# Kernel optimization log

Hardware: AMD Instinct MI355X
Metric: run time of the kernel (lower is better)

The kernel has to match this reference:

```python
import jax, jax.numpy as jnp
from jax import lax
import numpy as np


def _lap(cost):
    """Jonker-Volgenant shortest-augmenting-path LAP (same optimum as
    scipy.optimize.linear_sum_assignment) on cost [n, m] with n <= m.
    Returns for each row (0..n-1) the assigned column index."""
    n, m = cost.shape
    BIG = jnp.asarray(1e9, cost.dtype)
    a = jnp.pad(cost, ((1, 0), (1, 0)))  # 1-based rows/cols, [n+1, m+1]
    u = jnp.zeros(n + 1, cost.dtype)     # row duals
    v = jnp.zeros(m + 1, cost.dtype)     # col duals
    p = jnp.zeros(m + 1, jnp.int32)      # p[j] = row matched to col j (0 = free)

    def row_step(i, carry):
        u, v, p = carry
        p = p.at[0].set(i)  # virtual col 0 holds the row being inserted
        minv = jnp.full(m + 1, BIG, cost.dtype)
        used = jnp.zeros(m + 1, bool)
        way = jnp.zeros(m + 1, jnp.int32)

        def cond(s):
            u, v, p, way, minv, used, j0 = s
            return p[j0] != 0

        def body(s):
            u, v, p, way, minv, used, j0 = s
            used = used.at[j0].set(True)
            i0 = p[j0]
            cur = a[i0] - u[i0] - v                      # reduced costs, len m+1
            better = (cur < minv) & jnp.logical_not(used)
            minv = jnp.where(better, cur, minv)
            way = jnp.where(better, j0, way)
            masked = jnp.where(used, BIG, minv)
            j1 = jnp.argmin(masked).astype(jnp.int32)
            delta = masked[j1]
            u = u.at[p].add(jnp.where(used, delta, jnp.zeros((), cost.dtype)))
            v = jnp.where(used, v - delta, v)
            minv = jnp.where(used, minv, minv - delta)
            return (u, v, p, way, minv, used, j1)

        u, v, p, way, minv, used, j0 = lax.while_loop(
            cond, body, (u, v, p, way, minv, used, jnp.int32(0)))

        # backtrack the augmenting path
        def cond2(s):
            return s[1] != 0

        def body2(s):
            p, j0 = s
            j1 = way[j0]
            return (p.at[j0].set(p[j1]), j1)

        p, _ = lax.while_loop(cond2, body2, (p, j0))
        return (u, v, p)

    u, v, p = lax.fori_loop(1, n + 1, row_step, (u, v, p))
    # invert: row r (1-based) matched to col j  ->  ans[r-1] = j-1
    cols = jnp.arange(m + 1)
    valid = (p > 0) & (cols > 0)
    idx = jnp.where(valid, p - 1, n)  # invalid entries dumped into scratch slot n
    ans = jnp.zeros(n + 1, jnp.int32).at[idx].set((cols - 1).astype(jnp.int32))
    return ans[:n]


def _cdist_mm(x, y):
    """Batched euclidean cdist via the GEMM trick (torch use_mm_for_euclid_dist)."""
    x2 = jnp.sum(x * x, axis=-1)[..., :, None]   # [B, N, 1]
    y2 = jnp.sum(y * y, axis=-1)[..., None, :]   # [B, 1, M]
    xy = jnp.einsum('bnd,bmd->bnm', x, y)        # [B, N, M]
    return jnp.sqrt(jnp.maximum(x2 + y2 - 2.0 * xy, 0.0))


def setup_inputs() -> dict:
    key = jax.random.key(0)
    k1, k2 = jax.random.split(key)
    outputs = jax.random.normal(k1, (32, 512, 768), dtype=jnp.float32)
    targets = jax.random.normal(k2, (32, 200, 768), dtype=jnp.float32)
    return {"outputs": outputs, "targets": targets}


def reference(outputs, targets):
    # cost[b, n, m] = ||outputs[b, n] - targets[b, m]||_2  (block-diagonal slices
    # of the original cross-batch cdist are all that the matcher consumes)
    cost = _cdist_mm(outputs, targets)                       # [B, N, M]
    # solve with targets as rows (n=M <= m=N): pred column per gt row
    gt_to_pred = jax.vmap(_lap)(jnp.swapaxes(cost, 1, 2))    # [B, M]
    # scipy returns pred indices sorted ascending; replicate that ordering
    order = jnp.argsort(gt_to_pred, axis=1)                  # gt indices (index_j)
    index_i = jnp.take_along_axis(gt_to_pred, order, axis=1)
    index_j = order.astype(jnp.int32)
    return jnp.stack([index_i, index_j], axis=1)             # [B, 2, M] int32
```

## Files before the change

kernel.cpp:

```cpp
#include <hip/hip_runtime.h>
#include <math.h>

static constexpr int BATCH = 32;
static constexpr int NPRED = 512;
static constexpr int NTGT  = 200;
static constexpr int DIM   = 768;
#define BIGF  1e9f
#define USEDC 2e9f

__global__ __launch_bounds__(64) void row_norms_kernel(const float* __restrict__ x,
                                                       float* __restrict__ out) {
    int row = blockIdx.x;
    const float4* r = (const float4*)(x + (size_t)row * DIM);
    float s = 0.f;
#pragma unroll
    for (int k = 0; k < 3; ++k) {
        float4 v = r[threadIdx.x + 64 * k];
        s += v.x * v.x + v.y * v.y + v.z * v.z + v.w * v.w;
    }
#pragma unroll
    for (int off = 32; off; off >>= 1) s += __shfl_down(s, off);
    if (threadIdx.x == 0) out[row] = s;
}

__global__ __launch_bounds__(256) void cost_kernel(const float* __restrict__ O,
                                                   const float* __restrict__ T,
                                                   const float* __restrict__ no_arr,
                                                   const float* __restrict__ nt_arr,
                                                   float* __restrict__ cost) {
    const int b  = blockIdx.z;
    const int m0 = blockIdx.y * 32;
    const int n0 = blockIdx.x * 128;
    const float* Tb = T + (size_t)b * NTGT * DIM;
    const float* Ob = O + (size_t)b * NPRED * DIM;

    __shared__ float As[32][33];
    __shared__ float Bs[32][129];

    const int tid = threadIdx.x;
    const int tx = tid & 31;
    const int ty = tid >> 5;

    float acc[4][4] = {};

    for (int k0 = 0; k0 < DIM; k0 += 32) {
        {
            int ar = tid >> 3;
            int ak = (tid & 7) << 2;
            int gm = m0 + ar; if (gm > NTGT - 1) gm = NTGT - 1;
            float4 vA = *(const float4*)(Tb + (size_t)gm * DIM + k0 + ak);
            As[ak + 0][ar] = vA.x; As[ak + 1][ar] = vA.y;
            As[ak + 2][ar] = vA.z; As[ak + 3][ar] = vA.w;
        }
#pragma unroll
        for (int q = 0; q < 4; ++q) {
            int idx = q * 256 + tid;
            int br = idx >> 3;
            int bk = (idx & 7) << 2;
            float4 vB = *(const float4*)(Ob + (size_t)(n0 + br) * DIM + k0 + bk);
            Bs[bk + 0][br] = vB.x; Bs[bk + 1][br] = vB.y;
            Bs[bk + 2][br] = vB.z; Bs[bk + 3][br] = vB.w;
        }
        __syncthreads();
#pragma unroll
        for (int k = 0; k < 32; ++k) {
            float a0 = As[k][ty], a1 = As[k][ty + 8],
                  a2 = As[k][ty + 16], a3 = As[k][ty + 24];
            float b0 = Bs[k][tx],      b1 = Bs[k][tx + 32],
                  b2 = Bs[k][tx + 64], b3 = Bs[k][tx + 96];
            acc[0][0] += a0 * b0; acc[0][1] += a0 * b1; acc[0][2] += a0 * b2; acc[0][3] += a0 * b3;
            acc[1][0] += a1 * b0; acc[1][1] += a1 * b1; acc[1][2] += a1 * b2; acc[1][3] += a1 * b3;
            acc[2][0] += a2 * b0; acc[2][1] += a2 * b1; acc[2][2] += a2 * b2; acc[2][3] += a2 * b3;
            acc[3][0] += a3 * b0; acc[3][1] += a3 * b1; acc[3][2] += a3 * b2; acc[3][3] += a3 * b3;
        }
        __syncthreads();
    }

#pragma unroll
    for (int i = 0; i < 4; ++i) {
        int gm = m0 + ty + 8 * i;
        if (gm < NTGT) {
            float ntv = nt_arr[b * NTGT + gm];
#pragma unroll
            for (int j = 0; j < 4; ++j) {
                int gn = n0 + tx + 32 * j;
                float d2 = ntv + no_arr[b * NPRED + gn] - 2.0f * acc[i][j];
                cost[((size_t)b * NTGT + gm) * NPRED + gn] = sqrtf(fmaxf(d2, 0.0f));
            }
        }
    }
}

__device__ __forceinline__ int rl(int v, int l) {
    return __builtin_amdgcn_readlane(v, l);
}
__device__ __forceinline__ float rlf(float v, int l) {
    return __int_as_float(__builtin_amdgcn_readlane(__float_as_int(v), l));
}
__device__ __forceinline__ int sel8i(const int* a, int s) {
    int r = a[0];
#pragma unroll
    for (int k = 1; k < 8; ++k) r = (s == k) ? a[k] : r;
    return r;
}
__device__ __forceinline__ float sel8f(const float* a, int s) {
    float r = a[0];
#pragma unroll
    for (int k = 1; k < 8; ++k) r = (s == k) ? a[k] : r;
    return r;
}
__device__ __forceinline__ float dpp_min_f32(float x) {
    float t;
    t = __int_as_float(__builtin_amdgcn_update_dpp(__float_as_int(x), __float_as_int(x), 0x111, 0xF, 0xF, false)); x = fminf(x, t);
    t = __int_as_float(__builtin_amdgcn_update_dpp(__float_as_int(x), __float_as_int(x), 0x112, 0xF, 0xF, false)); x = fminf(x, t);
    t = __int_as_float(__builtin_amdgcn_update_dpp(__float_as_int(x), __float_as_int(x), 0x114, 0xF, 0xF, false)); x = fminf(x, t);
    t = __int_as_float(__builtin_amdgcn_update_dpp(__float_as_int(x), __float_as_int(x), 0x118, 0xF, 0xF, false)); x = fminf(x, t);
    t = __int_as_float(__builtin_amdgcn_update_dpp(__float_as_int(x), __float_as_int(x), 0x142, 0xF, 0xF, false)); x = fminf(x, t);
    t = __int_as_float(__builtin_amdgcn_update_dpp(__float_as_int(x), __float_as_int(x), 0x143, 0xF, 0xF, false)); x = fminf(x, t);
    return x;
}

__global__ __launch_bounds__(64) void lap_kernel(const float* __restrict__ cost,
                                                 int* __restrict__ out) {
    const int b = blockIdx.x;
    const int lane = threadIdx.x;
    const float* C = cost + (size_t)b * NTGT * NPRED;
    const float* Cl = C + lane * 8;

    __shared__ float u0[NTGT + 1];
    __shared__ int g2p[NTGT];

    for (int k = lane; k < NTGT + 1; k += 64) u0[k] = 0.f;

    float v[8], minv[8], up[8];
    int p_arr[8], way_arr[8];
#pragma unroll
    for (int q = 0; q < 8; ++q) {
        v[q] = 0.f; up[q] = 0.f; p_arr[q] = 0; way_arr[q] = 0;
    }
    __syncthreads();

    float4 ca = *(const float4*)(Cl);
    float4 cb = *(const float4*)(Cl + 4);

    for (int i = 1; i <= NTGT; ++i) {
#pragma unroll
        for (int q = 0; q < 8; ++q) minv[q] = BIGF;
        float uI = 0.f;
        float u_i0 = 0.f;
        int j0 = 0;
        int j1 = 0;

        for (int it = 0; it <= NPRED; ++it) {
            float c[8];
            c[0] = ca.x; c[1] = ca.y; c[2] = ca.z; c[3] = ca.w;
            c[4] = cb.x; c[5] = cb.y; c[6] = cb.z; c[7] = cb.w;

#pragma unroll
            for (int q = 0; q < 8; ++q) {
                float cur = (c[q] - u_i0) - v[q];
                bool usedq = (minv[q] == USEDC);
                float cure = usedq ? USEDC : cur;
                bool imp = cure < minv[q];
                minv[q] = imp ? cure : minv[q];
                way_arr[q] = imp ? j0 : way_arr[q];
            }

            float v01 = (minv[0] <= minv[1]) ? minv[0] : minv[1];
            int   q01 = (minv[0] <= minv[1]) ? 0 : 1;
            float v23 = (minv[2] <= minv[3]) ? minv[2] : minv[3];
            int   q23 = (minv[2] <= minv[3]) ? 2 : 3;
            float v45 = (minv[4] <= minv[5]) ? minv[4] : minv[5];
            int   q45 = (minv[4] <= minv[5]) ? 4 : 5;
            float v67 = (minv[6] <= minv[7]) ? minv[6] : minv[7];
            int   q67 = (minv[6] <= minv[7]) ? 6 : 7;
            float v03 = (v01 <= v23) ? v01 : v23;
            int   q03 = (v01 <= v23) ? q01 : q23;
            float v47 = (v45 <= v67) ? v45 : v67;
            int   q47 = (v45 <= v67) ? q45 : q67;
            float lval = (v03 <= v47) ? v03 : v47;
            int   lq   = (v03 <= v47) ? q03 : q47;

            int   psel = sel8i(p_arr, lq);
            float usel = sel8f(up, lq);

            float wmin = dpp_min_f32(lval);
            wmin = rlf(wmin, 63);
            unsigned long long mask = __ballot(lval == wmin);
            int w = (int)__builtin_ctzll(mask);
            int qw = rl(lq, w);
            int i0n = rl(psel, w);
            float u_n = rlf(usel, w);
            float delta = wmin;
            j1 = w * 8 + qw + 1;
            bool done = (i0n == 0);

            if (!done) {
                const float* Crow = Cl + (size_t)(i0n - 1) * NPRED;
                ca = *(const float4*)(Crow);
                cb = *(const float4*)(Crow + 4);
            }

            uI += delta;
#pragma unroll
            for (int q = 0; q < 8; ++q) {
                bool usedq = (minv[q] == USEDC);
                v[q]    = usedq ? (v[q] - delta) : v[q];
                up[q]   = usedq ? (up[q] + delta) : up[q];
                minv[q] = usedq ? minv[q] : (minv[q] - delta);
            }
            int j1m1 = j1 - 1;
#pragma unroll
            for (int q = 0; q < 8; ++q) {
                bool mine = (lane * 8 + q) == j1m1;
                minv[q] = mine ? USEDC : minv[q];
            }

            if (done) break;
            u_i0 = u_n;
            j0 = j1;
        }

        if (i < NTGT) {
            const float* Crow = Cl + (size_t)i * NPRED;
            ca = *(const float4*)(Crow);
            cb = *(const float4*)(Crow + 4);
        }

#pragma unroll
        for (int q = 0; q < 8; ++q) {
            bool usedq = (minv[q] == USEDC);
            if (usedq && p_arr[q] != 0) u0[p_arr[q]] = up[q];
        }
        if (lane == 0) u0[i] = uI;

        {
            int j = j1;
            for (int s = 0; s <= NPRED; ++s) {
                int ow = (j - 1) >> 3, oq = (j - 1) & 7;
                int wj = rl(sel8i(way_arr, oq), ow);
                int pOfW;
                if (wj == 0) {
                    pOfW = i;
                } else {
                    int ow2 = (wj - 1) >> 3, oq2 = (wj - 1) & 7;
                    pOfW = rl(sel8i(p_arr, oq2), ow2);
                }
#pragma unroll
                for (int q = 0; q < 8; ++q) {
                    bool mine = (lane == ow) && (q == oq);
                    p_arr[q] = mine ? pOfW : p_arr[q];
                }
                if (wj == 0) break;
                j = wj;
            }
        }

        __syncthreads();
#pragma unroll
        for (int q = 0; q < 8; ++q) up[q] = u0[p_arr[q]];
    }

#pragma unroll
    for (int q = 0; q < 8; ++q) {
        int r = p_arr[q];
        if (r > 0) g2p[r - 1] = lane * 8 + q;
    }
    __syncthreads();

    for (int t = lane; t < NTGT; t += 64) {
        int myv = g2p[t];
        int rank = 0;
        for (int l = 0; l < NTGT; ++l) rank += (g2p[l] < myv) ? 1 : 0;
        out[b * 2 * NTGT + rank] = myv;
        out[b * 2 * NTGT + NTGT + rank] = t;
    }
}

extern "C" void kernel_launch(void* const* d_in, const int* in_sizes, int n_in,
                              void* d_out, int out_size, void* d_ws, size_t ws_size,
                              hipStream_t stream) {
    const float* outputs = (const float*)d_in[0];
    const float* targets = (const float*)d_in[1];
    int* out = (int*)d_out;

    float* cost   = (float*)d_ws;
    float* no_arr = cost + (size_t)BATCH * NTGT * NPRED;
    float* nt_arr = no_arr + (size_t)BATCH * NPRED;

    row_norms_kernel<<<BATCH * NPRED, 64, 0, stream>>>(outputs, no_arr);
    row_norms_kernel<<<BATCH * NTGT, 64, 0, stream>>>(targets, nt_arr);
    cost_kernel<<<dim3(NPRED / 128, (NTGT + 31) / 32, BATCH), 256, 0, stream>>>(
        outputs, targets, no_arr, nt_arr, cost);
    lap_kernel<<<BATCH, 64, 0, stream>>>(cost, out);
}
```

Baseline: 877.1 us.

## Speculatively prefetch cost row of predicted next column in LAP loop

After each augmenting step, the kernel computes the current minimum of minv (before the next row's reduced costs are folded in) to guess the next column, and prefetches that column's matched-row costs into registers. If the real argmin matches the guess, the prefetched values are used and the dependent global load leaves the critical path. The cost is an extra tree reduction, DPP min, ballot and readlanes each iteration, plus wasted loads whenever the guess is wrong.

```diff
diff --git a/kernel.cpp b/kernel.cpp
--- a/kernel.cpp
+++ b/kernel.cpp
@@ -119,6 +119,22 @@
     t = __int_as_float(__builtin_amdgcn_update_dpp(__float_as_int(x), __float_as_int(x), 0x143, 0xF, 0xF, false)); x = fminf(x, t);
     return x;
 }
+__device__ __forceinline__ float tree8(const float* m, int& lq) {
+    float v01 = (m[0] <= m[1]) ? m[0] : m[1];
+    int   q01 = (m[0] <= m[1]) ? 0 : 1;
+    float v23 = (m[2] <= m[3]) ? m[2] : m[3];
+    int   q23 = (m[2] <= m[3]) ? 2 : 3;
+    float v45 = (m[4] <= m[5]) ? m[4] : m[5];
+    int   q45 = (m[4] <= m[5]) ? 4 : 5;
+    float v67 = (m[6] <= m[7]) ? m[6] : m[7];
+    int   q67 = (m[6] <= m[7]) ? 6 : 7;
+    float v03 = (v01 <= v23) ? v01 : v23;
+    int   q03 = (v01 <= v23) ? q01 : q23;
+    float v47 = (v45 <= v67) ? v45 : v67;
+    int   q47 = (v45 <= v67) ? q45 : q67;
+    lq = (v03 <= v47) ? q03 : q47;
+    return (v03 <= v47) ? v03 : v47;
+}
 
 __global__ __launch_bounds__(64) void lap_kernel(const float* __restrict__ cost,
                                                  int* __restrict__ out) {
@@ -142,6 +158,7 @@
 
     float4 ca = *(const float4*)(Cl);
     float4 cb = *(const float4*)(Cl + 4);
+    float4 sa = ca, sb = cb;
 
     for (int i = 1; i <= NTGT; ++i) {
 #pragma unroll
@@ -150,6 +167,7 @@
         float u_i0 = 0.f;
         int j0 = 0;
         int j1 = 0;
+        int spec_j = 0;
 
         for (int it = 0; it <= NPRED; ++it) {
             float c[8];
@@ -166,29 +184,14 @@
                 way_arr[q] = imp ? j0 : way_arr[q];
             }
 
-            float v01 = (minv[0] <= minv[1]) ? minv[0] : minv[1];
-            int   q01 = (minv[0] <= minv[1]) ? 0 : 1;
-            float v23 = (minv[2] <= minv[3]) ? minv[2] : minv[3];
-            int   q23 = (minv[2] <= minv[3]) ? 2 : 3;
-            float v45 = (minv[4] <= minv[5]) ? minv[4] : minv[5];
-            int   q45 = (minv[4] <= minv[5]) ? 4 : 5;
-            float v67 = (minv[6] <= minv[7]) ? minv[6] : minv[7];
-            int   q67 = (minv[6] <= minv[7]) ? 6 : 7;
-            float v03 = (v01 <= v23) ? v01 : v23;
-            int   q03 = (v01 <= v23) ? q01 : q23;
-            float v47 = (v45 <= v67) ? v45 : v67;
-            int   q47 = (v45 <= v67) ? q45 : q67;
-            float lval = (v03 <= v47) ? v03 : v47;
-            int   lq   = (v03 <= v47) ? q03 : q47;
-
+            int lq;
+            float lval = tree8(minv, lq);
             int   psel = sel8i(p_arr, lq);
             float usel = sel8f(up, lq);
-
-            float wmin = dpp_min_f32(lval);
-            wmin = rlf(wmin, 63);
+            float wmin = rlf(dpp_min_f32(lval), 63);
             unsigned long long mask = __ballot(lval == wmin);
             int w = (int)__builtin_ctzll(mask);
-            int qw = rl(lq, w);
+            int qw  = rl(lq, w);
             int i0n = rl(psel, w);
             float u_n = rlf(usel, w);
             float delta = wmin;
@@ -196,9 +199,13 @@
             bool done = (i0n == 0);
 
             if (!done) {
-                const float* Crow = Cl + (size_t)(i0n - 1) * NPRED;
-                ca = *(const float4*)(Crow);
-                cb = *(const float4*)(Crow + 4);
+                if (j1 == spec_j) {
+                    ca = sa; cb = sb;
+                } else {
+                    const float* Crow = Cl + (size_t)(i0n - 1) * NPRED;
+                    ca = *(const float4*)(Crow);
+                    cb = *(const float4*)(Crow + 4);
+                }
             }
 
             uI += delta;
@@ -217,6 +224,25 @@
             }
 
             if (done) break;
+
+            {
+                int lq2;
+                float l2 = tree8(minv, lq2);
+                int psel2 = sel8i(p_arr, lq2);
+                float w2v = rlf(dpp_min_f32(l2), 63);
+                unsigned long long m2 = __ballot(l2 == w2v);
+                int w2 = (int)__builtin_ctzll(m2);
+                int q2 = rl(lq2, w2);
+                int p2 = rl(psel2, w2);
+                int spec_new = w2 * 8 + q2 + 1;
+                if (p2 != 0 && spec_new != spec_j) {
+                    const float* Srow = Cl + (size_t)(p2 - 1) * NPRED;
+                    sa = *(const float4*)(Srow);
+                    sb = *(const float4*)(Srow + 4);
+                }
+                spec_j = spec_new;
+            }
+
             u_i0 = u_n;
             j0 = j1;
         }
```

New measurement: 879.6 us. Within noise of the previous version (+0.3%).
